# Kernel tuning notes

Measured on AMD Instinct MI355X. Metric: run time of the kernel, lower is better.

## Reference

```python
import jax, jax.numpy as jnp
import numpy as np

B, N, NIN = 32, 128, 64
MSG_HID, MSG_OUT, N_HID, N_OUT = 256, 64, 256, 64
E = N * (N - 1)  # fully connected, no self loops


def setup_inputs() -> dict:
    key = jax.random.key(0)
    ks = jax.random.split(key, 12)

    # one-hot incidence matrices (NRI convention)
    off = np.ones((N, N), dtype=np.float32) - np.eye(N, dtype=np.float32)
    recv_idx, send_idx = np.where(off)
    eye = np.eye(N, dtype=np.float32)
    rel_rec = jnp.asarray(eye[recv_idx])    # [E, N]
    rel_send = jnp.asarray(eye[send_idx])   # [E, N]

    s = 0.05
    inp = {
        "inputs": jax.random.normal(ks[0], (B, N, NIN), jnp.float32),
        "rel_rec": rel_rec,
        "rel_send": rel_send,
        "rel_types": jax.random.uniform(ks[1], (B, E, 2), jnp.float32),
        "msg_fc1_w": jax.random.normal(ks[2], (MSG_HID, 2 * NIN), jnp.float32) * s,
        "msg_fc1_b": jnp.zeros((MSG_HID,), jnp.float32),
        "msg_fc2_w": jax.random.normal(ks[3], (MSG_OUT, MSG_HID), jnp.float32) * s,
        "msg_fc2_b": jnp.zeros((MSG_OUT,), jnp.float32),
        "out_fc1_w": jax.random.normal(ks[4], (N_HID, MSG_OUT), jnp.float32) * s,
        "out_fc1_b": jnp.zeros((N_HID,), jnp.float32),
        "out_fc2_w": jax.random.normal(ks[5], (N_HID, N_HID), jnp.float32) * s,
        "out_fc2_b": jnp.zeros((N_HID,), jnp.float32),
        "out_fc3_w": jax.random.normal(ks[6], (N_OUT, N_HID), jnp.float32) * s,
        "out_fc3_b": jnp.zeros((N_OUT,), jnp.float32),
    }
    return inp


def reference(inputs, rel_rec, rel_send, rel_types,
              msg_fc1_w, msg_fc1_b, msg_fc2_w, msg_fc2_b,
              out_fc1_w, out_fc1_b, out_fc2_w, out_fc2_b,
              out_fc3_w, out_fc3_b):
    # node2edge: gather sender / receiver node features via one-hot matmul
    senders = jnp.einsum('en,bnf->bef', rel_send, inputs)    # [B,E,NIN]
    receivers = jnp.einsum('en,bnf->bef', rel_rec, inputs)   # [B,E,NIN]
    pre_msg = jnp.concatenate([senders, receivers], axis=-1)  # [B,E,2*NIN]

    all_msgs = jnp.zeros(pre_msg.shape[:2] + (MSG_OUT,), pre_msg.dtype)
    for i in range(2):  # edge-type loop (shared weights, as in the original)
        msg = jax.nn.relu(pre_msg @ msg_fc1_w.T + msg_fc1_b)
        msg = jax.nn.relu(msg @ msg_fc2_w.T + msg_fc2_b)
        all_msgs = all_msgs + msg * rel_types[:, :, i:i + 1]

    # edge2node: scatter-add messages to receiving nodes
    agg_msgs = jnp.einsum('bem,en->bnm', all_msgs, rel_rec)   # [B,N,MSG_OUT]

    pred = jax.nn.relu(agg_msgs @ out_fc1_w.T + out_fc1_b)
    pred = jax.nn.relu(pred @ out_fc2_w.T + out_fc2_b)
    pred = pred @ out_fc3_w.T + out_fc3_b                      # [B,N,N_OUT]
    return pred
```

## Files before the change

kernel.cpp:

```cpp
#include <hip/hip_runtime.h>

#define BB 32
#define NN_ 128
#define NIN 64
#define MH 256
#define MO 64
#define NH 256
#define NO 64
#define EDGES 16256

typedef _Float16 half8 __attribute__((ext_vector_type(8)));
typedef __attribute__((ext_vector_type(4))) float f32x4;
typedef __attribute__((ext_vector_type(16))) float f32x16;


static __device__ __forceinline__ unsigned short f2h(float f) {
    return __builtin_bit_cast(unsigned short, (_Float16)f);
}

static __device__ __forceinline__ half8 pack8h(float4 f0, float4 f1) {
    uint4 u;
    u.x = __builtin_bit_cast(unsigned, __builtin_amdgcn_cvt_pkrtz(f0.x, f0.y));
    u.y = __builtin_bit_cast(unsigned, __builtin_amdgcn_cvt_pkrtz(f0.z, f0.w));
    u.z = __builtin_bit_cast(unsigned, __builtin_amdgcn_cvt_pkrtz(f1.x, f1.y));
    u.w = __builtin_bit_cast(unsigned, __builtin_amdgcn_cvt_pkrtz(f1.z, f1.w));
    return __builtin_bit_cast(half8, u);
}

static __device__ __forceinline__ half8 addrelu(uint4 s, uint4 p) {
    half8 a = __builtin_bit_cast(half8, s) + __builtin_bit_cast(half8, p);
    half8 z = {};
    return __builtin_elementwise_max(a, z);
}

__global__ __launch_bounds__(256) void prep_kernel(
    const float* __restrict__ x, const float* __restrict__ W1,
    const float* __restrict__ b1, const float* __restrict__ W2,
    const float* __restrict__ O1, const float* __restrict__ O2,
    const float* __restrict__ O3,
    unsigned short* __restrict__ psb, unsigned short* __restrict__ prb,
    unsigned short* __restrict__ w2b, unsigned short* __restrict__ o1b,
    unsigned short* __restrict__ o2b, unsigned short* __restrict__ o3b)
{
    int blk = blockIdx.x;
    int t = threadIdx.x;
    if (blk < 256) {
        int row0 = blk << 4;
        int b = blk >> 3;
        int w = t >> 6, lane = t & 63, ml = lane & 15, q = lane >> 4;

        half8 aX[2];
        #pragma unroll
        for (int s = 0; s < 2; ++s) {
            const float* base = x + (size_t)(row0 + ml) * NIN + s * 32 + q * 8;
            aX[s] = pack8h(*(const float4*)base, *(const float4*)(base + 4));
        }

        #pragma unroll
        for (int half = 0; half < 2; ++half) {
            #pragma unroll
            for (int nt = 0; nt < 4; ++nt) {
                int col = w * 64 + nt * 16 + ml;
                const float* wrow = W1 + (size_t)col * (2 * NIN) + half * 64 + q * 8;
                f32x4 acc = (f32x4){0.f, 0.f, 0.f, 0.f};
                #pragma unroll
                for (int s = 0; s < 2; ++s) {
                    half8 bw = pack8h(*(const float4*)(wrow + 32 * s),
                                      *(const float4*)(wrow + 32 * s + 4));
                    acc = __builtin_amdgcn_mfma_f32_16x16x32_f16(aX[s], bw, acc, 0, 0, 0);
                }
                if (half == 0) {
                    #pragma unroll
                    for (int reg = 0; reg < 4; ++reg) {
                        int n = (row0 + q * 4 + reg) & 127;
                        psb[((size_t)(b * 32 + (col >> 3)) * NN_ + n) * 8 + (col & 7)]
                            = f2h(acc[reg]);
                    }
                } else {
                    float bv = b1[col];
                    #pragma unroll
                    for (int reg = 0; reg < 4; ++reg) {
                        int n = (row0 + q * 4 + reg) & 127;
                        prb[((size_t)(b * NN_) + n) * MH + col] = f2h(acc[reg] + bv);
                    }
                }
            }
        }
    } else if (blk < 320) {
        int i = ((blk - 256) << 8) + t;
        int kc4 = i >> 9, rem = i & 511;
        int n = rem >> 3, k7 = i & 7;
        w2b[i] = f2h(W2[n * MH + kc4 * 8 + k7]);
    } else {
        int i = ((blk - 320) << 8) + t;
        if (i < 16384)       o1b[i]         = f2h(O1[i]);
        else if (i < 81920)  o2b[i - 16384] = f2h(O2[i - 16384]);
        else                 o3b[i - 81920] = f2h(O3[i - 81920]);
    }
}

__global__ __launch_bounds__(512) void edge_node_kernel(
    const float* __restrict__ rt, const float* __restrict__ b2,
    const unsigned short* __restrict__ psb, const unsigned short* __restrict__ prb,
    const unsigned short* __restrict__ w2b,
    const unsigned short* __restrict__ o1b, const float* __restrict__ b1o,
    const unsigned short* __restrict__ o2b, const float* __restrict__ b2o,
    const unsigned short* __restrict__ o3b, const float* __restrict__ b3o,
    float* __restrict__ out)
{
    int blk = blockIdx.x;
    int t = threadIdx.x;
    int wv = t >> 6;
    int lane = t & 63;
    int ml = lane & 15, q = lane >> 4;
    int l31 = lane & 31, h = lane >> 5;
    int mt = wv >> 1;
    int nt2 = wv & 1;

    int b = blk >> 4;
    int rbase = (blk & 15) << 3;

    __shared__ uint4 w2L[2048];
    __shared__ float rtwA[4][2][128];
    __shared__ uint4 prL[8][32];
    __shared__ float aggL[16][68];
    __shared__ __align__(16) char uni[17280];
    typedef float red_t[2][4][64];
    red_t* redA = (red_t*)uni;
    typedef unsigned short row264[264];
    row264* h1L = (row264*)uni;
    row264* h2L = (row264*)(uni + 8448);

    {
        const uint4* w24 = (const uint4*)w2b;
        #pragma unroll
        for (int i = 0; i < 4; ++i)
            w2L[t + 512 * i] = w24[t + 512 * i];
    }
    if (t < 256) {
        int r = t >> 5, c = t & 31;
        prL[r][c] = ((const uint4*)(prb + ((size_t)(b * NN_ + rbase + r)) * MH))[c];
    }
    #pragma unroll
    for (int j = 0; j < 2; ++j) {
        int idx = 2 * t + j;
        int un = idx >> 8, rr = (idx >> 7) & 1, s = idx & 127;
        int r = rbase + un * 2 + rr;
        float v = 0.f;
        if (s != r) {
            int e = r * 127 + s - (s > r ? 1 : 0);
            const float* p = rt + ((size_t)(b * EDGES + e)) * 2;
            v = p[0] + p[1];
        }
        rtwA[un][rr][s] = v;
    }

    aggL[8 + wv][lane] = 0.f;

    float b2v = b2[32 * nt2 + l31];

    uint4 usr[16];
    {
        const uint4* ps4 = (const uint4*)psb + (size_t)b * (32 * NN_);
        #pragma unroll
        for (int ks = 0; ks < 16; ++ks)
            usr[ks] = ps4[(2 * ks + h) * NN_ + 32 * mt + l31];
    }

    __syncthreads();

    #pragma unroll 1
    for (int un = 0; un < 4; ++un) {
        f32x16 acc0 = {0.f,0.f,0.f,0.f,0.f,0.f,0.f,0.f,
                       0.f,0.f,0.f,0.f,0.f,0.f,0.f,0.f};
        f32x16 acc1 = acc0;

        #pragma unroll
        for (int ks = 0; ks < 16; ++ks) {
            uint4 up0 = prL[un * 2][2 * ks + h];
            uint4 up1 = prL[un * 2 + 1][2 * ks + h];
            half8 a0 = addrelu(usr[ks], up0);
            half8 a1 = addrelu(usr[ks], up1);
            half8 bw = __builtin_bit_cast(half8,
                           w2L[(2 * ks + h) * 64 + 32 * nt2 + l31]);
            acc0 = __builtin_amdgcn_mfma_f32_32x32x16_f16(a0, bw, acc0, 0, 0, 0);
            acc1 = __builtin_amdgcn_mfma_f32_32x32x16_f16(a1, bw, acc1, 0, 0, 0);
        }

        float cs0 = 0.f, cs1 = 0.f;
        #pragma unroll
        for (int reg = 0; reg < 16; ++reg) {
            int row = 32 * mt + (reg & 3) + 8 * (reg >> 2) + 4 * h;
            cs0 += fmaxf(acc0[reg] + b2v, 0.f) * rtwA[un][0][row];
            cs1 += fmaxf(acc1[reg] + b2v, 0.f) * rtwA[un][1][row];
        }
        cs0 += __shfl_xor(cs0, 32);
        cs1 += __shfl_xor(cs1, 32);
        if (lane < 32) {
            redA[un][0][mt][32 * nt2 + l31] = cs0;
            redA[un][1][mt][32 * nt2 + l31] = cs1;
        }
    }

    __syncthreads();
    {
        int row = t >> 6, o = t & 63;
        float s = 0.f;
        #pragma unroll
        for (int m4 = 0; m4 < 4; ++m4) s += redA[row >> 1][row & 1][m4][o];
        aggL[row][o] = s;
    }
    __syncthreads();

    half8 aA[2];
    #pragma unroll
    for (int s = 0; s < 2; ++s) {
        const float* base = &aggL[ml][32 * s + q * 8];
        aA[s] = pack8h(*(const float4*)base, *(const float4*)(base + 4));
    }

    #pragma unroll
    for (int nt = 0; nt < 2; ++nt) {
        int ntg = wv * 2 + nt;
        f32x4 acc = (f32x4){0.f, 0.f, 0.f, 0.f};
        #pragma unroll
        for (int s = 0; s < 2; ++s) {
            half8 bw = *(const half8*)(o1b + (size_t)(ntg * 16 + ml) * 64 + 32 * s + q * 8);
            acc = __builtin_amdgcn_mfma_f32_16x16x32_f16(aA[s], bw, acc, 0, 0, 0);
        }
        float bv = b1o[ntg * 16 + ml];
        #pragma unroll
        for (int reg = 0; reg < 4; ++reg)
            h1L[q * 4 + reg][ntg * 16 + ml] = f2h(fmaxf(acc[reg] + bv, 0.f));
    }
    __syncthreads();

    half8 aH[8];
    #pragma unroll
    for (int ks = 0; ks < 8; ++ks)
        aH[ks] = *(const half8*)&h1L[ml][32 * ks + q * 8];
    #pragma unroll
    for (int nt = 0; nt < 2; ++nt) {
        int ntg = wv * 2 + nt;
        const unsigned short* wrow = o2b + (size_t)(ntg * 16 + ml) * NH + q * 8;
        f32x4 acc = (f32x4){0.f, 0.f, 0.f, 0.f};
        #pragma unroll
        for (int ks = 0; ks < 8; ++ks) {
            half8 bw = *(const half8*)(wrow + 32 * ks);
            acc = __builtin_amdgcn_mfma_f32_16x16x32_f16(aH[ks], bw, acc, 0, 0, 0);
        }
        float bv = b2o[ntg * 16 + ml];
        #pragma unroll
        for (int reg = 0; reg < 4; ++reg)
            h2L[q * 4 + reg][ntg * 16 + ml] = f2h(fmaxf(acc[reg] + bv, 0.f));
    }
    __syncthreads();

    if (wv < 4) {
        #pragma unroll
        for (int ks = 0; ks < 8; ++ks)
            aH[ks] = *(const half8*)&h2L[ml][32 * ks + q * 8];
        const unsigned short* wrow = o3b + (size_t)(wv * 16 + ml) * NH + q * 8;
        f32x4 acc = (f32x4){0.f, 0.f, 0.f, 0.f};
        #pragma unroll
        for (int ks = 0; ks < 8; ++ks) {
            half8 bw = *(const half8*)(wrow + 32 * ks);
            acc = __builtin_amdgcn_mfma_f32_16x16x32_f16(aH[ks], bw, acc, 0, 0, 0);
        }
        float bv = b3o[wv * 16 + ml];
        if (q < 2) {
            #pragma unroll
            for (int reg = 0; reg < 4; ++reg)
                out[(size_t)(b * NN_ + rbase + q * 4 + reg) * NO + wv * 16 + ml]
                    = acc[reg] + bv;
        }
    }
}

extern "C" void kernel_launch(void* const* d_in, const int* in_sizes, int n_in,
                              void* d_out, int out_size, void* d_ws, size_t ws_size,
                              hipStream_t stream) {
    const float* x   = (const float*)d_in[0];
    const float* rt  = (const float*)d_in[3];
    const float* W1  = (const float*)d_in[4];
    const float* b1  = (const float*)d_in[5];
    const float* W2  = (const float*)d_in[6];
    const float* b2  = (const float*)d_in[7];
    const float* O1  = (const float*)d_in[8];
    const float* b1o = (const float*)d_in[9];
    const float* O2  = (const float*)d_in[10];
    const float* b2o = (const float*)d_in[11];
    const float* O3  = (const float*)d_in[12];
    const float* b3o = (const float*)d_in[13];

    float* ws  = (float*)d_ws;
    unsigned short* psb = (unsigned short*)ws;
    unsigned short* prb = (unsigned short*)(ws + 524288);
    unsigned short* w2b = (unsigned short*)(ws + 1048576);
    unsigned short* o1b = (unsigned short*)(ws + 1056768);
    unsigned short* o2b = (unsigned short*)(ws + 1064960);
    unsigned short* o3b = (unsigned short*)(ws + 1097728);
    float* out = (float*)d_out;

    hipLaunchKernelGGL(prep_kernel, dim3(704), dim3(256), 0, stream,
                       x, W1, b1, W2, O1, O2, O3, psb, prb, w2b, o1b, o2b, o3b);
    hipLaunchKernelGGL(edge_node_kernel, dim3(512), dim3(512), 0, stream,
                       rt, b2, psb, prb, w2b, o1b, b1o, o2b, b2o, o3b, b3o, out);
}
```

Measured before the change: 128.1 us.

## Fuse prep kernel into edge-node kernel and compute node projections in-block

Removes the separate prep kernel and its fp16 workspace round-trip. Each block now computes its own sender and receiver projections of x through W1 with MFMA, reshuffling the sender results into the register layout the edge loop expects via cross-lane shuffles. All weights (W2, O1-O3) are converted from fp32 on the fly as they are loaded. This drops one launch and a global write/read pass, in exchange for redundant sender-projection work in every block (16 blocks per batch) and extra fp32 weight traffic.

```diff
diff --git a/kernel.cpp b/kernel.cpp
--- a/kernel.cpp
+++ b/kernel.cpp
@@ -13,7 +13,6 @@
 typedef __attribute__((ext_vector_type(4))) float f32x4;
 typedef __attribute__((ext_vector_type(16))) float f32x16;
 
-
 static __device__ __forceinline__ unsigned short f2h(float f) {
     return __builtin_bit_cast(unsigned short, (_Float16)f);
 }
@@ -27,85 +26,23 @@
     return __builtin_bit_cast(half8, u);
 }
 
+static __device__ __forceinline__ half8 pload(const float* p) {
+    return pack8h(*(const float4*)p, *(const float4*)(p + 4));
+}
+
 static __device__ __forceinline__ half8 addrelu(uint4 s, uint4 p) {
     half8 a = __builtin_bit_cast(half8, s) + __builtin_bit_cast(half8, p);
     half8 z = {};
     return __builtin_elementwise_max(a, z);
 }
 
-__global__ __launch_bounds__(256) void prep_kernel(
+__global__ __launch_bounds__(512) void fused_kernel(
     const float* __restrict__ x, const float* __restrict__ W1,
     const float* __restrict__ b1, const float* __restrict__ W2,
-    const float* __restrict__ O1, const float* __restrict__ O2,
-    const float* __restrict__ O3,
-    unsigned short* __restrict__ psb, unsigned short* __restrict__ prb,
-    unsigned short* __restrict__ w2b, unsigned short* __restrict__ o1b,
-    unsigned short* __restrict__ o2b, unsigned short* __restrict__ o3b)
-{
-    int blk = blockIdx.x;
-    int t = threadIdx.x;
-    if (blk < 256) {
-        int row0 = blk << 4;
-        int b = blk >> 3;
-        int w = t >> 6, lane = t & 63, ml = lane & 15, q = lane >> 4;
-
-        half8 aX[2];
-        #pragma unroll
-        for (int s = 0; s < 2; ++s) {
-            const float* base = x + (size_t)(row0 + ml) * NIN + s * 32 + q * 8;
-            aX[s] = pack8h(*(const float4*)base, *(const float4*)(base + 4));
-        }
-
-        #pragma unroll
-        for (int half = 0; half < 2; ++half) {
-            #pragma unroll
-            for (int nt = 0; nt < 4; ++nt) {
-                int col = w * 64 + nt * 16 + ml;
-                const float* wrow = W1 + (size_t)col * (2 * NIN) + half * 64 + q * 8;
-                f32x4 acc = (f32x4){0.f, 0.f, 0.f, 0.f};
-                #pragma unroll
-                for (int s = 0; s < 2; ++s) {
-                    half8 bw = pack8h(*(const float4*)(wrow + 32 * s),
-                                      *(const float4*)(wrow + 32 * s + 4));
-                    acc = __builtin_amdgcn_mfma_f32_16x16x32_f16(aX[s], bw, acc, 0, 0, 0);
-                }
-                if (half == 0) {
-                    #pragma unroll
-                    for (int reg = 0; reg < 4; ++reg) {
-                        int n = (row0 + q * 4 + reg) & 127;
-                        psb[((size_t)(b * 32 + (col >> 3)) * NN_ + n) * 8 + (col & 7)]
-                            = f2h(acc[reg]);
-                    }
-                } else {
-                    float bv = b1[col];
-                    #pragma unroll
-                    for (int reg = 0; reg < 4; ++reg) {
-                        int n = (row0 + q * 4 + reg) & 127;
-                        prb[((size_t)(b * NN_) + n) * MH + col] = f2h(acc[reg] + bv);
-                    }
-                }
-            }
-        }
-    } else if (blk < 320) {
-        int i = ((blk - 256) << 8) + t;
-        int kc4 = i >> 9, rem = i & 511;
-        int n = rem >> 3, k7 = i & 7;
-        w2b[i] = f2h(W2[n * MH + kc4 * 8 + k7]);
-    } else {
-        int i = ((blk - 320) << 8) + t;
-        if (i < 16384)       o1b[i]         = f2h(O1[i]);
-        else if (i < 81920)  o2b[i - 16384] = f2h(O2[i - 16384]);
-        else                 o3b[i - 81920] = f2h(O3[i - 81920]);
-    }
-}
-
-__global__ __launch_bounds__(512) void edge_node_kernel(
     const float* __restrict__ rt, const float* __restrict__ b2,
-    const unsigned short* __restrict__ psb, const unsigned short* __restrict__ prb,
-    const unsigned short* __restrict__ w2b,
-    const unsigned short* __restrict__ o1b, const float* __restrict__ b1o,
-    const unsigned short* __restrict__ o2b, const float* __restrict__ b2o,
-    const unsigned short* __restrict__ o3b, const float* __restrict__ b3o,
+    const float* __restrict__ O1, const float* __restrict__ b1o,
+    const float* __restrict__ O2, const float* __restrict__ b2o,
+    const float* __restrict__ O3, const float* __restrict__ b3o,
     float* __restrict__ out)
 {
     int blk = blockIdx.x;
@@ -122,7 +59,7 @@
 
     __shared__ uint4 w2L[2048];
     __shared__ float rtwA[4][2][128];
-    __shared__ uint4 prL[8][32];
+    __shared__ unsigned short prLh[8][256];
     __shared__ float aggL[16][68];
     __shared__ __align__(16) char uni[17280];
     typedef float red_t[2][4][64];
@@ -131,15 +68,12 @@
     row264* h1L = (row264*)uni;
     row264* h2L = (row264*)(uni + 8448);
 
-    {
-        const uint4* w24 = (const uint4*)w2b;
-        #pragma unroll
-        for (int i = 0; i < 4; ++i)
-            w2L[t + 512 * i] = w24[t + 512 * i];
-    }
-    if (t < 256) {
-        int r = t >> 5, c = t & 31;
-        prL[r][c] = ((const uint4*)(prb + ((size_t)(b * NN_ + rbase + r)) * MH))[c];
+    #pragma unroll
+    for (int ii = 0; ii < 4; ++ii) {
+        int i = t + 512 * ii;
+        int kc4 = i >> 6, col = i & 63;
+        const float* p = W2 + (size_t)col * MH + kc4 * 8;
+        w2L[i] = __builtin_bit_cast(uint4, pload(p));
     }
     #pragma unroll
     for (int j = 0; j < 2; ++j) {
@@ -154,20 +88,67 @@
         }
         rtwA[un][rr][s] = v;
     }
-
     aggL[8 + wv][lane] = 0.f;
 
-    float b2v = b2[32 * nt2 + l31];
+    {
+        f32x16 D = {};
+        int xr = b * NN_ + rbase + (l31 & 7);
+        #pragma unroll
+        for (int kk = 0; kk < 4; ++kk) {
+            half8 bf = pload(x + (size_t)xr * NIN + 16 * kk + 8 * h);
+            half8 af = pload(W1 + (size_t)(32 * wv + l31) * (2 * NIN) + NIN
+                             + 16 * kk + 8 * h);
+            D = __builtin_amdgcn_mfma_f32_32x32x16_f16(af, bf, D, 0, 0, 0);
+        }
+        if (l31 < 8) {
+            #pragma unroll
+            for (int reg = 0; reg < 16; ++reg) {
+                int u = 32 * wv + (reg & 3) + 8 * (reg >> 2) + 4 * h;
+                prLh[l31][u] = f2h(D[reg] + b1[u]);
+            }
+        }
+    }
 
     uint4 usr[16];
     {
-        const uint4* ps4 = (const uint4*)psb + (size_t)b * (32 * NN_);
-        #pragma unroll
-        for (int ks = 0; ks < 16; ++ks)
-            usr[ks] = ps4[(2 * ks + h) * NN_ + 32 * mt + l31];
-    }
-
-    __syncthreads();
+        half8 xB[4];
+        int sr = b * NN_ + 32 * mt + l31;
+        #pragma unroll
+        for (int kk = 0; kk < 4; ++kk)
+            xB[kk] = pload(x + (size_t)sr * NIN + 16 * kk + 8 * h);
+
+        #pragma unroll
+        for (int ut = 0; ut < 8; ++ut) {
+            f32x16 D = {};
+            #pragma unroll
+            for (int kk = 0; kk < 4; ++kk) {
+                half8 af = pload(W1 + (size_t)(32 * ut + l31) * (2 * NIN)
+                                 + 16 * kk + 8 * h);
+                D = __builtin_amdgcn_mfma_f32_32x32x16_f16(af, xB[kk], D, 0, 0, 0);
+            }
+            unsigned g[8], xg[8];
+            #pragma unroll
+            for (int p = 0; p < 8; ++p)
+                g[p] = __builtin_bit_cast(unsigned,
+                         __builtin_amdgcn_cvt_pkrtz(D[2 * p], D[2 * p + 1]));
+            #pragma unroll
+            for (int p = 0; p < 8; ++p)
+                xg[p] = __shfl_xor(g[p], 32);
+            uint4 u0, u1;
+            u0.x = h ? xg[2] : g[0];  u0.y = h ? xg[3] : g[1];
+            u0.z = h ? g[2]  : xg[0]; u0.w = h ? g[3]  : xg[1];
+            u1.x = h ? xg[6] : g[4];  u1.y = h ? xg[7] : g[5];
+            u1.z = h ? g[6]  : xg[4]; u1.w = h ? g[7]  : xg[5];
+            usr[2 * ut] = u0;
+            usr[2 * ut + 1] = u1;
+        }
+    }
+
+    float b2v = b2[32 * nt2 + l31];
+
+    __syncthreads();
+
+    const uint4* prL4 = (const uint4*)prLh;
 
     #pragma unroll 1
     for (int un = 0; un < 4; ++un) {
@@ -177,8 +158,8 @@
 
         #pragma unroll
         for (int ks = 0; ks < 16; ++ks) {
-            uint4 up0 = prL[un * 2][2 * ks + h];
-            uint4 up1 = prL[un * 2 + 1][2 * ks + h];
+            uint4 up0 = prL4[(un * 2) * 32 + 2 * ks + h];
+            uint4 up1 = prL4[(un * 2 + 1) * 32 + 2 * ks + h];
             half8 a0 = addrelu(usr[ks], up0);
             half8 a1 = addrelu(usr[ks], up1);
             half8 bw = __builtin_bit_cast(half8,
@@ -225,7 +206,7 @@
         f32x4 acc = (f32x4){0.f, 0.f, 0.f, 0.f};
         #pragma unroll
         for (int s = 0; s < 2; ++s) {
-            half8 bw = *(const half8*)(o1b + (size_t)(ntg * 16 + ml) * 64 + 32 * s + q * 8);
+            half8 bw = pload(O1 + (size_t)(ntg * 16 + ml) * MO + 32 * s + q * 8);
             acc = __builtin_amdgcn_mfma_f32_16x16x32_f16(aA[s], bw, acc, 0, 0, 0);
         }
         float bv = b1o[ntg * 16 + ml];
@@ -242,11 +223,11 @@
     #pragma unroll
     for (int nt = 0; nt < 2; ++nt) {
         int ntg = wv * 2 + nt;
-        const unsigned short* wrow = o2b + (size_t)(ntg * 16 + ml) * NH + q * 8;
+        const float* wrow = O2 + (size_t)(ntg * 16 + ml) * NH + q * 8;
         f32x4 acc = (f32x4){0.f, 0.f, 0.f, 0.f};
         #pragma unroll
         for (int ks = 0; ks < 8; ++ks) {
-            half8 bw = *(const half8*)(wrow + 32 * ks);
+            half8 bw = pload(wrow + 32 * ks);
             acc = __builtin_amdgcn_mfma_f32_16x16x32_f16(aH[ks], bw, acc, 0, 0, 0);
         }
         float bv = b2o[ntg * 16 + ml];
@@ -260,11 +241,11 @@
         #pragma unroll
         for (int ks = 0; ks < 8; ++ks)
             aH[ks] = *(const half8*)&h2L[ml][32 * ks + q * 8];
-        const unsigned short* wrow = o3b + (size_t)(wv * 16 + ml) * NH + q * 8;
+        const float* wrow = O3 + (size_t)(wv * 16 + ml) * NH + q * 8;
         f32x4 acc = (f32x4){0.f, 0.f, 0.f, 0.f};
         #pragma unroll
         for (int ks = 0; ks < 8; ++ks) {
-            half8 bw = *(const half8*)(wrow + 32 * ks);
+            half8 bw = pload(wrow + 32 * ks);
             acc = __builtin_amdgcn_mfma_f32_16x16x32_f16(aH[ks], bw, acc, 0, 0, 0);
         }
         float bv = b3o[wv * 16 + ml];
@@ -292,18 +273,9 @@
     const float* b2o = (const float*)d_in[11];
     const float* O3  = (const float*)d_in[12];
     const float* b3o = (const float*)d_in[13];
-
-    float* ws  = (float*)d_ws;
-    unsigned short* psb = (unsigned short*)ws;
-    unsigned short* prb = (unsigned short*)(ws + 524288);
-    unsigned short* w2b = (unsigned short*)(ws + 1048576);
-    unsigned short* o1b = (unsigned short*)(ws + 1056768);
-    unsigned short* o2b = (unsigned short*)(ws + 1064960);
-    unsigned short* o3b = (unsigned short*)(ws + 1097728);
     float* out = (float*)d_out;
-
-    hipLaunchKernelGGL(prep_kernel, dim3(704), dim3(256), 0, stream,
-                       x, W1, b1, W2, O1, O2, O3, psb, prb, w2b, o1b, o2b, o3b);
-    hipLaunchKernelGGL(edge_node_kernel, dim3(512), dim3(512), 0, stream,
-                       rt, b2, psb, prb, w2b, o1b, b1o, o2b, b2o, o3b, b3o, out);
-}
+    (void)d_ws; (void)ws_size;
+
+    hipLaunchKernelGGL(fused_kernel, dim3(512), dim3(512), 0, stream,
+                       x, W1, b1, W2, rt, b2, O1, b1o, O2, b2o, O3, b3o, out);
+}
```

After: 173.4 us. 1.35x slower.
